# Kernel tuning notes

Hardware: AMD Instinct MI355X
Metric: run time of the kernel (lower is better)

Reference implementation:

```python
import jax, jax.numpy as jnp
import numpy as np

N_NODES = 100000
N_EDGES = 1600000
SZ_IN = 128
DIM_I = 1024


def setup_inputs() -> dict:
    key = jax.random.key(0)
    k1, k2, k3, k4, k5 = jax.random.split(key, 5)
    x = jax.random.normal(k1, (N_NODES, SZ_IN), dtype=jnp.float32)
    edge_index = jax.random.randint(k2, (2, N_EDGES), 0, N_NODES, dtype=jnp.int64)
    # torch Linear weight is [out_features, in_features]
    agg_W = jax.random.normal(k3, (SZ_IN, SZ_IN), dtype=jnp.float32) / np.sqrt(SZ_IN)
    agg_b = jnp.zeros((SZ_IN,), dtype=jnp.float32)
    lin_W = jax.random.normal(k4, (DIM_I, 2 * SZ_IN), dtype=jnp.float32) / np.sqrt(2 * SZ_IN)
    return {"x": x, "edge_index": edge_index, "agg_W": agg_W, "agg_b": agg_b, "lin_W": lin_W}


def reference(x, edge_index, agg_W, agg_b, lin_W):
    # GraphSAGE layer, depth=1, agg='max', concat=True, training mode (no self-loop/dropout edits).
    u, v = edge_index[0], edge_index[1]
    n = x.shape[0]
    # gather neighbor features, linear + ReLU  -> [E, sz_in]
    msg = jax.nn.relu(x[v] @ agg_W.T + agg_b)
    # scatter-max per target node; torch_scatter initializes out to zeros,
    # so missing nodes get 0 and all results are max(values, 0)
    hn = jnp.maximum(jax.ops.segment_max(msg, u, num_segments=n), 0.0)
    # concat + linear (no bias) + ReLU -> [N, dim_i]
    h = jax.nn.relu(jnp.concatenate([x, hn], axis=1) @ lin_W.T)
    return h
```

## Files before the change

kernel.cpp:

```cpp
#include <hip/hip_runtime.h>
#include <hip/hip_bf16.h>

typedef __attribute__((ext_vector_type(8))) short short8;
typedef __attribute__((ext_vector_type(4))) float f32x4;

__device__ __forceinline__ float bfu2f(unsigned short u) {
    unsigned int x = ((unsigned int)u) << 16;
    float f;
    __builtin_memcpy(&f, &x, 4);
    return f;
}
__device__ __forceinline__ unsigned short f2bfu(float f) {
    unsigned int x;
    __builtin_memcpy(&x, &f, 4);
    unsigned int r = (x + 0x7FFFu + ((x >> 16) & 1u)) >> 16;
    return (unsigned short)r;
}

__device__ __forceinline__ void gload_lds16(const void* g, void* l) {
    __builtin_amdgcn_global_load_lds(
        (const __attribute__((address_space(1))) void*)g,
        (__attribute__((address_space(3))) void*)l, 16, 0, 0);
}

#define BM 128
#define BN 128
#define BK 32
#define LDA 32
#define BCAP 64

template<bool F32OUT>
__device__ __forceinline__ void gemm_tile(
    const unsigned short* __restrict__ Alo,
    const unsigned short* __restrict__ Ahi,
    const unsigned short* __restrict__ B,
    const float* __restrict__ bias,
    void* __restrict__ Cv,
    int M, int N, int K, int relu, int m0, int n0,
    unsigned short* As, unsigned short* Bs)
{
    const int tid  = threadIdx.x;
    const int lane = tid & 63;
    const int wave = tid >> 6;
    const int wr   = wave >> 1;
    const int wc   = wave & 1;
    const int fm   = lane & 15;
    const int fq   = lane >> 4;

    f32x4 acc[4][4] = {};

    const int wbase = tid & ~63;

    for (int k0 = 0; k0 < K; k0 += BK) {
        __syncthreads();
        const unsigned short* Ab = (k0 < 128) ? Alo : Ahi;
        const int ka = (k0 < 128) ? k0 : (k0 - 128);
        #pragma unroll
        for (int i = 0; i < 2; ++i) {
            int c  = i * 256 + tid;
            int r  = c >> 2;
            int c8 = (c & 3) << 3;
            int grow = m0 + r;
            if (grow >= M) grow = M - 1;
            gload_lds16(Ab + (size_t)grow * 128 + ka + c8,
                        &As[(i * 256 + wbase) * 8]);
            gload_lds16(B + (size_t)(n0 + r) * K + k0 + c8,
                        &Bs[(i * 256 + wbase) * 8]);
        }
        __syncthreads();

        short8 af[4], bf[4];
        #pragma unroll
        for (int i = 0; i < 4; ++i)
            af[i] = *(const short8*)(&As[(wr * 64 + i * 16 + fm) * LDA + fq * 8]);
        #pragma unroll
        for (int j = 0; j < 4; ++j)
            bf[j] = *(const short8*)(&Bs[(wc * 64 + j * 16 + fm) * LDA + fq * 8]);

        #pragma unroll
        for (int i = 0; i < 4; ++i)
            #pragma unroll
            for (int j = 0; j < 4; ++j)
                acc[i][j] = __builtin_amdgcn_mfma_f32_16x16x32_bf16(
                                af[i], bf[j], acc[i][j], 0, 0, 0);
    }

    #pragma unroll
    for (int i = 0; i < 4; ++i) {
        #pragma unroll
        for (int r = 0; r < 4; ++r) {
            int gm = m0 + wr * 64 + i * 16 + fq * 4 + r;
            if (gm < M) {
                #pragma unroll
                for (int j = 0; j < 4; ++j) {
                    int gn = n0 + wc * 64 + j * 16 + fm;
                    float val = acc[i][j][r];
                    if (bias) val += bias[gn];
                    if (relu) val = fmaxf(val, 0.0f);
                    if (F32OUT)
                        __builtin_nontemporal_store(val,
                            &((float*)Cv)[(size_t)gm * N + gn]);
                    else
                        ((unsigned short*)Cv)[(size_t)gm * N + gn] = f2bfu(val);
                }
            }
        }
    }
}

template<bool F32OUT>
__global__ __launch_bounds__(256, 2)
void gemm_bt(const unsigned short* __restrict__ Alo,
             const unsigned short* __restrict__ Ahi,
             const unsigned short* __restrict__ B,
             const float* __restrict__ bias,
             void* __restrict__ Cv,
             int M, int N, int K, int relu)
{
    __shared__ unsigned short As[BM * LDA];
    __shared__ unsigned short Bs[BN * LDA];

    const int nwg  = gridDim.x * gridDim.y;
    int lid = blockIdx.y * gridDim.x + blockIdx.x;
    int wg  = lid;
    if ((nwg & 7) == 0) {
        int cpx = nwg >> 3;
        wg = (lid & 7) * cpx + (lid >> 3);
    }
    const int m0 = (wg / gridDim.x) * BM;
    const int n0 = (wg % gridDim.x) * BN;
    gemm_tile<F32OUT>(Alo, Ahi, B, bias, Cv, M, N, K, relu, m0, n0, As, Bs);
}

__global__ __launch_bounds__(256, 2)
void gemm1_fill_k(const unsigned short* __restrict__ xb,
                  const unsigned short* __restrict__ awb,
                  const float* __restrict__ bias,
                  unsigned short* __restrict__ y, int M, int MT,
                  const int* __restrict__ ei, int* __restrict__ cnt,
                  int* __restrict__ adj, int E)
{
    __shared__ unsigned short As[BM * LDA];
    __shared__ unsigned short Bs[BN * LDA];

    int b = blockIdx.x;
    if (b < MT) {
        gemm_tile<false>(xb, xb, awb, bias, y, M, 128, 128, 0, b * BM, 0, As, Bs);
        return;
    }
    int e = ((b - MT) * 256 + (int)threadIdx.x) * 4;
    if (e >= E) return;
    if (e + 3 < E) {
        int4 u = *(const int4*)(ei + e);
        int4 v = *(const int4*)(ei + E + e);
        int p0 = atomicAdd(&cnt[u.x], 1);
        int p1 = atomicAdd(&cnt[u.y], 1);
        int p2 = atomicAdd(&cnt[u.z], 1);
        int p3 = atomicAdd(&cnt[u.w], 1);
        if (p0 < BCAP) adj[((size_t)u.x << 6) + p0] = v.x;
        if (p1 < BCAP) adj[((size_t)u.y << 6) + p1] = v.y;
        if (p2 < BCAP) adj[((size_t)u.z << 6) + p2] = v.z;
        if (p3 < BCAP) adj[((size_t)u.w << 6) + p3] = v.w;
    } else {
        for (int j = 0; j < 4 && e + j < E; ++j) {
            int u = ei[e + j], v = ei[E + e + j];
            int p = atomicAdd(&cnt[u], 1);
            if (p < BCAP) adj[((size_t)u << 6) + p] = v;
        }
    }
}

__device__ __forceinline__ void cvt4(const float* __restrict__ src,
                                     unsigned short* __restrict__ dst, int t)
{
    float4 f = ((const float4*)src)[t];
    ushort4 o;
    o.x = f2bfu(f.x); o.y = f2bfu(f.y); o.z = f2bfu(f.z); o.w = f2bfu(f.w);
    ((ushort4*)dst)[t] = o;
}

__global__ __launch_bounds__(256)
void prep_k(const float* __restrict__ x, unsigned short* __restrict__ xb, int n4x,
            const float* __restrict__ aW, unsigned short* __restrict__ awb, int n4a,
            const float* __restrict__ lW, unsigned short* __restrict__ lwb, int n4l,
            int* __restrict__ cnt, int n4d)
{
    int t = blockIdx.x * 256 + threadIdx.x;
    if (t < n4x) { cvt4(x, xb, t); return; }
    t -= n4x;
    if (t < n4a) { cvt4(aW, awb, t); return; }
    t -= n4a;
    if (t < n4l) { cvt4(lW, lwb, t); return; }
    t -= n4l;
    if (t < n4d) ((int4*)cnt)[t] = make_int4(0, 0, 0, 0);
}

__global__ __launch_bounds__(256)
void gather_max_k(const int* __restrict__ cnt, const int* __restrict__ adj,
                  const unsigned short* __restrict__ y,
                  unsigned short* __restrict__ hnb, int NN)
{
    int t = blockIdx.x * 256 + threadIdx.x;
    int u = t >> 4;
    if (u >= NN) return;
    int c = (t & 15) << 3;
    const unsigned short* yc = y + c;
    int n = cnt[u];
    if (n > BCAP) n = BCAP;
    const int* bucket = adj + ((size_t)u << 6);
    short8 a0 = {0, 0, 0, 0, 0, 0, 0, 0};
    short8 a1 = {0, 0, 0, 0, 0, 0, 0, 0};
    int i = 0;
    for (; i + 3 < n; i += 4) {
        int v0 = bucket[i], v1 = bucket[i + 1], v2 = bucket[i + 2], v3 = bucket[i + 3];
        short8 y0 = *(const short8*)(yc + (size_t)v0 * 128);
        short8 y1 = *(const short8*)(yc + (size_t)v1 * 128);
        short8 y2 = *(const short8*)(yc + (size_t)v2 * 128);
        short8 y3 = *(const short8*)(yc + (size_t)v3 * 128);
        a0 = __builtin_elementwise_max(a0, y0);
        a1 = __builtin_elementwise_max(a1, y1);
        a0 = __builtin_elementwise_max(a0, y2);
        a1 = __builtin_elementwise_max(a1, y3);
    }
    for (; i < n; ++i) {
        short8 y0 = *(const short8*)(yc + (size_t)bucket[i] * 128);
        a0 = __builtin_elementwise_max(a0, y0);
    }
    a0 = __builtin_elementwise_max(a0, a1);
    *(short8*)(hnb + (size_t)u * 128 + c) = a0;
}

extern "C" void kernel_launch(void* const* d_in, const int* in_sizes, int n_in,
                              void* d_out, int out_size, void* d_ws, size_t ws_size,
                              hipStream_t stream)
{
    const float* x     = (const float*)d_in[0];
    const int*   ei    = (const int*)d_in[1];
    const float* agg_W = (const float*)d_in[2];
    const float* agg_b = (const float*)d_in[3];
    const float* lin_W = (const float*)d_in[4];
    float*       out   = (float*)d_out;

    const int NN = in_sizes[0] / 128;
    const int E  = in_sizes[1] / 2;
    const int DI = in_sizes[4] / 256;

    char* ws = (char*)d_ws;
    const size_t xN = (size_t)NN * 128;
    unsigned short* xb  = (unsigned short*)ws;
    unsigned short* y   = xb + xN;
    unsigned short* hnb = y + xN;
    unsigned short* awb = hnb + xN;
    unsigned short* lwb = awb + 128 * 128;
    char* p = (char*)(lwb + (size_t)DI * 256);
    int* cnt = (int*)p;
    int* adj = cnt + NN;

    const int MT = (NN + BM - 1) / BM;
    const int FB = (E / 4 + 255) / 256;

    const int n4x = (int)(xN / 4);
    const int n4a = 128 * 128 / 4;
    const int n4l = DI * 256 / 4;
    const int n4d = (NN + 3) / 4;
    {
        long long tot = (long long)n4x + n4a + n4l + n4d;
        prep_k<<<(int)((tot + 255) / 256), 256, 0, stream>>>(
            x, xb, n4x, agg_W, awb, n4a, lin_W, lwb, n4l, cnt, n4d);
    }

    gemm1_fill_k<<<MT + FB, 256, 0, stream>>>(xb, awb, agg_b, y, NN, MT,
                                              ei, cnt, adj, E);

    {
        long long threads = (long long)NN * 16;
        int blocks = (int)((threads + 255) / 256);
        gather_max_k<<<blocks, 256, 0, stream>>>(cnt, adj, y, hnb, NN);
    }

    gemm_bt<true><<<dim3(DI / BN, MT), 256, 0, stream>>>(xb, hnb, lwb, nullptr, out, NN, DI, 256, 1);
}
```

Before: 640.1 us.

## Replace final GEMM with 256x256-tile, 8-phase pipelined MFMA kernel

The output GEMM (N×256 by 256×1024, fp32 output) moves from the generic 128x128 tiled kernel to a dedicated 512-thread kernel. It uses 256x256 tiles, XOR-swizzled LDS with direct global-to-LDS loads, and an unrolled 8-phase schedule that overlaps staging of the next K-slice with MFMA work, using explicit waitcnt, barriers and setprio. The goal is more data reuse per tile and hiding of global-load latency in the dominant GEMM. In exchange the code is much more complex, LDS use per block rises, and the schedule is hardcoded for K=256.

```diff
diff --git a/kernel.cpp b/kernel.cpp
--- a/kernel.cpp
+++ b/kernel.cpp
@@ -48,7 +48,6 @@
     const int fq   = lane >> 4;
 
     f32x4 acc[4][4] = {};
-
     const int wbase = tid & ~63;
 
     for (int k0 = 0; k0 < K; k0 += BK) {
@@ -106,30 +105,6 @@
             }
         }
     }
-}
-
-template<bool F32OUT>
-__global__ __launch_bounds__(256, 2)
-void gemm_bt(const unsigned short* __restrict__ Alo,
-             const unsigned short* __restrict__ Ahi,
-             const unsigned short* __restrict__ B,
-             const float* __restrict__ bias,
-             void* __restrict__ Cv,
-             int M, int N, int K, int relu)
-{
-    __shared__ unsigned short As[BM * LDA];
-    __shared__ unsigned short Bs[BN * LDA];
-
-    const int nwg  = gridDim.x * gridDim.y;
-    int lid = blockIdx.y * gridDim.x + blockIdx.x;
-    int wg  = lid;
-    if ((nwg & 7) == 0) {
-        int cpx = nwg >> 3;
-        wg = (lid & 7) * cpx + (lid >> 3);
-    }
-    const int m0 = (wg / gridDim.x) * BM;
-    const int n0 = (wg % gridDim.x) * BN;
-    gemm_tile<F32OUT>(Alo, Ahi, B, bias, Cv, M, N, K, relu, m0, n0, As, Bs);
 }
 
 __global__ __launch_bounds__(256, 2)
@@ -168,6 +143,186 @@
             if (p < BCAP) adj[((size_t)u << 6) + p] = v;
         }
     }
+}
+
+#define BM2 256
+#define BN2 256
+
+__device__ __forceinline__ void stage_unit(const unsigned short* __restrict__ src,
+                                           int stride, int row0, int rmax,
+                                           unsigned short* dst, int tid)
+{
+    #pragma unroll
+    for (int j = 0; j < 2; ++j) {
+        int c = j * 512 + tid;
+        int r = c >> 3;
+        int s = (c & 7) ^ (r & 7);
+        int grow = row0 + r;
+        if (grow > rmax) grow = rmax;
+        gload_lds16(src + (size_t)grow * stride + s * 8,
+                    dst + (size_t)(j * 512 + (tid & ~63)) * 8);
+    }
+}
+
+__device__ __forceinline__ short8 frag_ld(const unsigned short* base, int row,
+                                          int ks, int fq)
+{
+    int cb = (ks * 64 + fq * 16) ^ ((row & 7) << 4);
+    return *(const short8*)((const char*)(base + row * 64) + cb);
+}
+
+__device__ __forceinline__ void load_a4(short8 (&a)[4][2],
+    const unsigned short* base, int wr, int fm, int fq)
+{
+    #pragma unroll
+    for (int mi = 0; mi < 4; ++mi)
+        #pragma unroll
+        for (int ks = 0; ks < 2; ++ks)
+            a[mi][ks] = frag_ld(base, wr * 64 + mi * 16 + fm, ks, fq);
+}
+__device__ __forceinline__ void load_b2(short8 (&bb)[2][2],
+    const unsigned short* base, int wc, int fm, int fq)
+{
+    #pragma unroll
+    for (int nj = 0; nj < 2; ++nj)
+        #pragma unroll
+        for (int ks = 0; ks < 2; ++ks)
+            bb[nj][ks] = frag_ld(base, wc * 32 + nj * 16 + fm, ks, fq);
+}
+
+#define PH_MID() do { \
+    __builtin_amdgcn_s_barrier(); \
+    asm volatile("s_waitcnt lgkmcnt(0)" ::: "memory"); \
+    __builtin_amdgcn_sched_barrier(0); \
+    __builtin_amdgcn_s_setprio(1); \
+} while (0)
+#define PH_END() do { \
+    __builtin_amdgcn_s_setprio(0); \
+    __builtin_amdgcn_s_barrier(); \
+    asm volatile("" ::: "memory"); \
+} while (0)
+
+template<int QM, int QN>
+__device__ __forceinline__ void do_mfma(f32x4 (&acc)[2][4][2][2],
+                                        short8 (&a)[4][2], short8 (&b)[2][2][2])
+{
+    #pragma unroll
+    for (int mi = 0; mi < 4; ++mi)
+        #pragma unroll
+        for (int nj = 0; nj < 2; ++nj)
+            #pragma unroll
+            for (int ks = 0; ks < 2; ++ks)
+                acc[QM][mi][QN][nj] = __builtin_amdgcn_mfma_f32_16x16x32_bf16(
+                    a[mi][ks], b[QN][nj][ks], acc[QM][mi][QN][nj], 0, 0, 0);
+}
+
+__global__ __launch_bounds__(512, 2)
+void gemm3_8ph(const unsigned short* __restrict__ xb,
+               const unsigned short* __restrict__ hnb,
+               const unsigned short* __restrict__ lwb,
+               float* __restrict__ out, int M, int N)
+{
+    __shared__ unsigned short lds[2][2][2][128 * 64];
+
+    const int tid = threadIdx.x;
+    const int nx  = gridDim.x;
+    const int nwg = nx * gridDim.y;
+    int orig = blockIdx.y * nx + blockIdx.x;
+    int q = nwg >> 3, r8 = nwg & 7;
+    int xcd = orig & 7, pos = orig >> 3;
+    int wg = (xcd < r8 ? xcd * (q + 1) : r8 * (q + 1) + (xcd - r8) * q) + pos;
+    const int m0 = (wg / nx) * BM2;
+    const int n0 = (wg % nx) * BN2;
+
+    const int lane = tid & 63;
+    const int wave = tid >> 6;
+    const int wr = wave >> 2;
+    const int wc = wave & 3;
+    const int fm = lane & 15;
+    const int fq = lane >> 4;
+    const int rmaxA = M - 1;
+    const int rmaxB = N - 1;
+
+    f32x4 acc[2][4][2][2] = {};
+    short8 a[4][2];
+    short8 b[2][2][2];
+
+    stage_unit(xb,        128, m0,        rmaxA, &lds[0][0][0][0], tid);
+    stage_unit(lwb,       256, n0,        rmaxB, &lds[0][1][0][0], tid);
+    stage_unit(lwb,       256, n0 + 128,  rmaxB, &lds[0][1][1][0], tid);
+    stage_unit(xb,        128, m0 + 128,  rmaxA, &lds[0][0][1][0], tid);
+    stage_unit(xb + 64,   128, m0,        rmaxA, &lds[1][0][0][0], tid);
+    stage_unit(lwb + 64,  256, n0,        rmaxB, &lds[1][1][0][0], tid);
+    stage_unit(lwb + 64,  256, n0 + 128,  rmaxB, &lds[1][1][1][0], tid);
+    asm volatile("s_waitcnt vmcnt(6)" ::: "memory");
+    __builtin_amdgcn_s_barrier();
+    asm volatile("" ::: "memory");
+
+    #pragma unroll
+    for (int it = 0; it < 2; ++it) {
+        const unsigned short* AT1 = (it == 0) ? xb + 64 : hnb + 64;
+
+        load_a4(a, &lds[0][0][0][0], wr, fm, fq);
+        load_b2(b[0], &lds[0][1][0][0], wc, fm, fq);
+        stage_unit(AT1, 128, m0 + 128, rmaxA, &lds[1][0][1][0], tid);
+        PH_MID(); do_mfma<0, 0>(acc, a, b); PH_END();
+
+        load_b2(b[1], &lds[0][1][1][0], wc, fm, fq);
+        if (it == 0) stage_unit(hnb, 128, m0, rmaxA, &lds[0][0][0][0], tid);
+        PH_MID(); do_mfma<0, 1>(acc, a, b); PH_END();
+
+        load_a4(a, &lds[0][0][1][0], wr, fm, fq);
+        if (it == 0) stage_unit(lwb + 128, 256, n0, rmaxB, &lds[0][1][0][0], tid);
+        PH_MID(); do_mfma<1, 0>(acc, a, b); PH_END();
+
+        if (it == 0) stage_unit(lwb + 128, 256, n0 + 128, rmaxB, &lds[0][1][1][0], tid);
+        PH_MID(); do_mfma<1, 1>(acc, a, b);
+        __builtin_amdgcn_s_setprio(0);
+        if (it == 0) asm volatile("s_waitcnt vmcnt(6)" ::: "memory");
+        else         asm volatile("s_waitcnt vmcnt(0)" ::: "memory");
+        __builtin_amdgcn_s_barrier();
+        asm volatile("" ::: "memory");
+
+        load_a4(a, &lds[1][0][0][0], wr, fm, fq);
+        load_b2(b[0], &lds[1][1][0][0], wc, fm, fq);
+        if (it == 0) stage_unit(hnb, 128, m0 + 128, rmaxA, &lds[0][0][1][0], tid);
+        PH_MID(); do_mfma<0, 0>(acc, a, b); PH_END();
+
+        load_b2(b[1], &lds[1][1][1][0], wc, fm, fq);
+        if (it == 0) stage_unit(hnb + 64, 128, m0, rmaxA, &lds[1][0][0][0], tid);
+        PH_MID(); do_mfma<0, 1>(acc, a, b); PH_END();
+
+        load_a4(a, &lds[1][0][1][0], wr, fm, fq);
+        if (it == 0) stage_unit(lwb + 192, 256, n0, rmaxB, &lds[1][1][0][0], tid);
+        PH_MID(); do_mfma<1, 0>(acc, a, b); PH_END();
+
+        if (it == 0) stage_unit(lwb + 192, 256, n0 + 128, rmaxB, &lds[1][1][1][0], tid);
+        PH_MID(); do_mfma<1, 1>(acc, a, b);
+        __builtin_amdgcn_s_setprio(0);
+        if (it == 0) asm volatile("s_waitcnt vmcnt(6)" ::: "memory");
+        __builtin_amdgcn_s_barrier();
+        asm volatile("" ::: "memory");
+    }
+
+    #pragma unroll
+    for (int qm = 0; qm < 2; ++qm)
+        #pragma unroll
+        for (int mi = 0; mi < 4; ++mi)
+            #pragma unroll
+            for (int rr = 0; rr < 4; ++rr) {
+                int gm = m0 + qm * 128 + wr * 64 + mi * 16 + fq * 4 + rr;
+                if (gm < M) {
+                    #pragma unroll
+                    for (int qn = 0; qn < 2; ++qn)
+                        #pragma unroll
+                        for (int nj = 0; nj < 2; ++nj) {
+                            int gn = n0 + qn * 128 + wc * 32 + nj * 16 + fm;
+                            float v = fmaxf(acc[qm][mi][qn][nj][rr], 0.0f);
+                            __builtin_nontemporal_store(v,
+                                &out[(size_t)gm * N + gn]);
+                        }
+                }
+            }
 }
 
 __device__ __forceinline__ void cvt4(const float* __restrict__ src,
@@ -278,5 +433,8 @@
         gather_max_k<<<blocks, 256, 0, stream>>>(cnt, adj, y, hnb, NN);
     }
 
-    gemm_bt<true><<<dim3(DI / BN, MT), 256, 0, stream>>>(xb, hnb, lwb, nullptr, out, NN, DI, 256, 1);
-}
+    {
+        dim3 g(DI / BN2, (NN + BM2 - 1) / BM2);
+        gemm3_8ph<<<g, 512, 0, stream>>>(xb, hnb, lwb, out, NN, DI);
+    }
+}
```

New measurement: 664.1 us. 1.04x slower.

## Fuse neighbor max-gather into final GEMM and drop hn buffer

Applied to the files above, without the earlier changes.

Removes the separate gather_max kernel and the hn intermediate: each block of the final GEMM gathers neighbor maxima for its 128 rows directly into LDS alongside the x tile, then sweeps all output column tiles reusing the A operand. The lin_W bf16 conversion is moved into the gemm1/fill launch. This saves a launch and an intermediate write and read. It risks lower occupancy from large LDS use and reduced parallelism, since one block now does all N tiles serially after a latency-bound gather.

```diff
diff --git a/kernel.cpp b/kernel.cpp
--- a/kernel.cpp
+++ b/kernel.cpp
@@ -4,12 +4,6 @@
 typedef __attribute__((ext_vector_type(8))) short short8;
 typedef __attribute__((ext_vector_type(4))) float f32x4;
 
-__device__ __forceinline__ float bfu2f(unsigned short u) {
-    unsigned int x = ((unsigned int)u) << 16;
-    float f;
-    __builtin_memcpy(&f, &x, 4);
-    return f;
-}
 __device__ __forceinline__ unsigned short f2bfu(float f) {
     unsigned int x;
     __builtin_memcpy(&x, &f, 4);
@@ -29,15 +23,12 @@
 #define LDA 32
 #define BCAP 64
 
-template<bool F32OUT>
-__device__ __forceinline__ void gemm_tile(
-    const unsigned short* __restrict__ Alo,
-    const unsigned short* __restrict__ Ahi,
+__device__ __forceinline__ void gemm_tile_bf16out(
+    const unsigned short* __restrict__ A,
     const unsigned short* __restrict__ B,
     const float* __restrict__ bias,
-    void* __restrict__ Cv,
-    int M, int N, int K, int relu, int m0, int n0,
-    unsigned short* As, unsigned short* Bs)
+    unsigned short* __restrict__ C,
+    int M, int m0, unsigned short* As, unsigned short* Bs)
 {
     const int tid  = threadIdx.x;
     const int lane = tid & 63;
@@ -48,13 +39,10 @@
     const int fq   = lane >> 4;
 
     f32x4 acc[4][4] = {};
-
     const int wbase = tid & ~63;
 
-    for (int k0 = 0; k0 < K; k0 += BK) {
+    for (int k0 = 0; k0 < 128; k0 += BK) {
         __syncthreads();
-        const unsigned short* Ab = (k0 < 128) ? Alo : Ahi;
-        const int ka = (k0 < 128) ? k0 : (k0 - 128);
         #pragma unroll
         for (int i = 0; i < 2; ++i) {
             int c  = i * 256 + tid;
@@ -62,9 +50,9 @@
             int c8 = (c & 3) << 3;
             int grow = m0 + r;
             if (grow >= M) grow = M - 1;
-            gload_lds16(Ab + (size_t)grow * 128 + ka + c8,
+            gload_lds16(A + (size_t)grow * 128 + k0 + c8,
                         &As[(i * 256 + wbase) * 8]);
-            gload_lds16(B + (size_t)(n0 + r) * K + k0 + c8,
+            gload_lds16(B + (size_t)r * 128 + k0 + c8,
                         &Bs[(i * 256 + wbase) * 8]);
         }
         __syncthreads();
@@ -93,43 +81,22 @@
             if (gm < M) {
                 #pragma unroll
                 for (int j = 0; j < 4; ++j) {
-                    int gn = n0 + wc * 64 + j * 16 + fm;
-                    float val = acc[i][j][r];
-                    if (bias) val += bias[gn];
-                    if (relu) val = fmaxf(val, 0.0f);
-                    if (F32OUT)
-                        __builtin_nontemporal_store(val,
-                            &((float*)Cv)[(size_t)gm * N + gn]);
-                    else
-                        ((unsigned short*)Cv)[(size_t)gm * N + gn] = f2bfu(val);
+                    int gn = wc * 64 + j * 16 + fm;
+                    float val = acc[i][j][r] + bias[gn];
+                    C[(size_t)gm * 128 + gn] = f2bfu(val);
                 }
             }
         }
     }
 }
 
-template<bool F32OUT>
-__global__ __launch_bounds__(256, 2)
-void gemm_bt(const unsigned short* __restrict__ Alo,
-             const unsigned short* __restrict__ Ahi,
-             const unsigned short* __restrict__ B,
-             const float* __restrict__ bias,
-             void* __restrict__ Cv,
-             int M, int N, int K, int relu)
-{
-    __shared__ unsigned short As[BM * LDA];
-    __shared__ unsigned short Bs[BN * LDA];
-
-    const int nwg  = gridDim.x * gridDim.y;
-    int lid = blockIdx.y * gridDim.x + blockIdx.x;
-    int wg  = lid;
-    if ((nwg & 7) == 0) {
-        int cpx = nwg >> 3;
-        wg = (lid & 7) * cpx + (lid >> 3);
-    }
-    const int m0 = (wg / gridDim.x) * BM;
-    const int n0 = (wg % gridDim.x) * BN;
-    gemm_tile<F32OUT>(Alo, Ahi, B, bias, Cv, M, N, K, relu, m0, n0, As, Bs);
+__device__ __forceinline__ void cvt4(const float* __restrict__ src,
+                                     unsigned short* __restrict__ dst, int t)
+{
+    float4 f = ((const float4*)src)[t];
+    ushort4 o;
+    o.x = f2bfu(f.x); o.y = f2bfu(f.y); o.z = f2bfu(f.z); o.w = f2bfu(f.w);
+    ((ushort4*)dst)[t] = o;
 }
 
 __global__ __launch_bounds__(256, 2)
@@ -138,51 +105,48 @@
                   const float* __restrict__ bias,
                   unsigned short* __restrict__ y, int M, int MT,
                   const int* __restrict__ ei, int* __restrict__ cnt,
-                  int* __restrict__ adj, int E)
+                  int* __restrict__ adj, int E, int FB,
+                  const float* __restrict__ lW,
+                  unsigned short* __restrict__ lwb, int n4l)
 {
     __shared__ unsigned short As[BM * LDA];
     __shared__ unsigned short Bs[BN * LDA];
 
     int b = blockIdx.x;
     if (b < MT) {
-        gemm_tile<false>(xb, xb, awb, bias, y, M, 128, 128, 0, b * BM, 0, As, Bs);
+        gemm_tile_bf16out(xb, awb, bias, y, M, b * BM, As, Bs);
         return;
     }
-    int e = ((b - MT) * 256 + (int)threadIdx.x) * 4;
-    if (e >= E) return;
-    if (e + 3 < E) {
-        int4 u = *(const int4*)(ei + e);
-        int4 v = *(const int4*)(ei + E + e);
-        int p0 = atomicAdd(&cnt[u.x], 1);
-        int p1 = atomicAdd(&cnt[u.y], 1);
-        int p2 = atomicAdd(&cnt[u.z], 1);
-        int p3 = atomicAdd(&cnt[u.w], 1);
-        if (p0 < BCAP) adj[((size_t)u.x << 6) + p0] = v.x;
-        if (p1 < BCAP) adj[((size_t)u.y << 6) + p1] = v.y;
-        if (p2 < BCAP) adj[((size_t)u.z << 6) + p2] = v.z;
-        if (p3 < BCAP) adj[((size_t)u.w << 6) + p3] = v.w;
-    } else {
-        for (int j = 0; j < 4 && e + j < E; ++j) {
-            int u = ei[e + j], v = ei[E + e + j];
-            int p = atomicAdd(&cnt[u], 1);
-            if (p < BCAP) adj[((size_t)u << 6) + p] = v;
-        }
-    }
-}
-
-__device__ __forceinline__ void cvt4(const float* __restrict__ src,
-                                     unsigned short* __restrict__ dst, int t)
-{
-    float4 f = ((const float4*)src)[t];
-    ushort4 o;
-    o.x = f2bfu(f.x); o.y = f2bfu(f.y); o.z = f2bfu(f.z); o.w = f2bfu(f.w);
-    ((ushort4*)dst)[t] = o;
+    if (b < MT + FB) {
+        int e = ((b - MT) * 256 + (int)threadIdx.x) * 4;
+        if (e >= E) return;
+        if (e + 3 < E) {
+            int4 u = *(const int4*)(ei + e);
+            int4 v = *(const int4*)(ei + E + e);
+            int p0 = atomicAdd(&cnt[u.x], 1);
+            int p1 = atomicAdd(&cnt[u.y], 1);
+            int p2 = atomicAdd(&cnt[u.z], 1);
+            int p3 = atomicAdd(&cnt[u.w], 1);
+            if (p0 < BCAP) adj[((size_t)u.x << 6) + p0] = v.x;
+            if (p1 < BCAP) adj[((size_t)u.y << 6) + p1] = v.y;
+            if (p2 < BCAP) adj[((size_t)u.z << 6) + p2] = v.z;
+            if (p3 < BCAP) adj[((size_t)u.w << 6) + p3] = v.w;
+        } else {
+            for (int j = 0; j < 4 && e + j < E; ++j) {
+                int u = ei[e + j], v = ei[E + e + j];
+                int p = atomicAdd(&cnt[u], 1);
+                if (p < BCAP) adj[((size_t)u << 6) + p] = v;
+            }
+        }
+        return;
+    }
+    int t = (b - MT - FB) * 256 + (int)threadIdx.x;
+    if (t < n4l) cvt4(lW, lwb, t);
 }
 
 __global__ __launch_bounds__(256)
 void prep_k(const float* __restrict__ x, unsigned short* __restrict__ xb, int n4x,
             const float* __restrict__ aW, unsigned short* __restrict__ awb, int n4a,
-            const float* __restrict__ lW, unsigned short* __restrict__ lwb, int n4l,
             int* __restrict__ cnt, int n4d)
 {
     int t = blockIdx.x * 256 + threadIdx.x;
@@ -190,44 +154,131 @@
     t -= n4x;
     if (t < n4a) { cvt4(aW, awb, t); return; }
     t -= n4a;
-    if (t < n4l) { cvt4(lW, lwb, t); return; }
-    t -= n4l;
     if (t < n4d) ((int4*)cnt)[t] = make_int4(0, 0, 0, 0);
 }
 
-__global__ __launch_bounds__(256)
-void gather_max_k(const int* __restrict__ cnt, const int* __restrict__ adj,
-                  const unsigned short* __restrict__ y,
-                  unsigned short* __restrict__ hnb, int NN)
-{
-    int t = blockIdx.x * 256 + threadIdx.x;
-    int u = t >> 4;
-    if (u >= NN) return;
-    int c = (t & 15) << 3;
-    const unsigned short* yc = y + c;
-    int n = cnt[u];
-    if (n > BCAP) n = BCAP;
-    const int* bucket = adj + ((size_t)u << 6);
-    short8 a0 = {0, 0, 0, 0, 0, 0, 0, 0};
-    short8 a1 = {0, 0, 0, 0, 0, 0, 0, 0};
-    int i = 0;
-    for (; i + 3 < n; i += 4) {
-        int v0 = bucket[i], v1 = bucket[i + 1], v2 = bucket[i + 2], v3 = bucket[i + 3];
-        short8 y0 = *(const short8*)(yc + (size_t)v0 * 128);
-        short8 y1 = *(const short8*)(yc + (size_t)v1 * 128);
-        short8 y2 = *(const short8*)(yc + (size_t)v2 * 128);
-        short8 y3 = *(const short8*)(yc + (size_t)v3 * 128);
-        a0 = __builtin_elementwise_max(a0, y0);
-        a1 = __builtin_elementwise_max(a1, y1);
-        a0 = __builtin_elementwise_max(a0, y2);
-        a1 = __builtin_elementwise_max(a1, y3);
-    }
-    for (; i < n; ++i) {
-        short8 y0 = *(const short8*)(yc + (size_t)bucket[i] * 128);
-        a0 = __builtin_elementwise_max(a0, y0);
-    }
-    a0 = __builtin_elementwise_max(a0, a1);
-    *(short8*)(hnb + (size_t)u * 128 + c) = a0;
+__global__ __launch_bounds__(256, 2)
+void gemm3_fused(const unsigned short* __restrict__ xb,
+                 const unsigned short* __restrict__ lwb,
+                 const int* __restrict__ cnt,
+                 const int* __restrict__ adj,
+                 const unsigned short* __restrict__ y,
+                 float* __restrict__ out, int M, int N)
+{
+    __shared__ unsigned short Ah[8][128 * 32];
+    __shared__ unsigned short Bs[128 * 32];
+
+    const int tid = threadIdx.x;
+    const int m0  = blockIdx.x * 128;
+    const int wbase = tid & ~63;
+
+    #pragma unroll
+    for (int kc = 0; kc < 4; ++kc) {
+        #pragma unroll
+        for (int i = 0; i < 2; ++i) {
+            int c  = i * 256 + tid;
+            int r  = c >> 2;
+            int c8 = (c & 3) << 3;
+            int grow = m0 + r;
+            if (grow >= M) grow = M - 1;
+            gload_lds16(xb + (size_t)grow * 128 + kc * 32 + c8,
+                        &Ah[kc][(i * 256 + wbase) * 8]);
+        }
+    }
+
+    {
+        int g   = tid >> 4;
+        int ch  = (tid & 15) << 3;
+        int kc  = 4 + (ch >> 5);
+        int col = ch & 31;
+        const unsigned short* yc = y + ch;
+        for (int p = 0; p < 8; ++p) {
+            int r = p * 16 + g;
+            int u = m0 + r;
+            short8 a0 = {0, 0, 0, 0, 0, 0, 0, 0};
+            short8 a1 = {0, 0, 0, 0, 0, 0, 0, 0};
+            if (u < M) {
+                int n = cnt[u];
+                if (n > BCAP) n = BCAP;
+                const int* bucket = adj + ((size_t)u << 6);
+                int i = 0;
+                for (; i + 3 < n; i += 4) {
+                    int v0 = bucket[i],     v1 = bucket[i + 1];
+                    int v2 = bucket[i + 2], v3 = bucket[i + 3];
+                    short8 y0 = *(const short8*)(yc + (size_t)v0 * 128);
+                    short8 y1 = *(const short8*)(yc + (size_t)v1 * 128);
+                    short8 y2 = *(const short8*)(yc + (size_t)v2 * 128);
+                    short8 y3 = *(const short8*)(yc + (size_t)v3 * 128);
+                    a0 = __builtin_elementwise_max(a0, y0);
+                    a1 = __builtin_elementwise_max(a1, y1);
+                    a0 = __builtin_elementwise_max(a0, y2);
+                    a1 = __builtin_elementwise_max(a1, y3);
+                }
+                for (; i < n; ++i) {
+                    short8 y0 = *(const short8*)(yc + (size_t)bucket[i] * 128);
+                    a0 = __builtin_elementwise_max(a0, y0);
+                }
+            }
+            a0 = __builtin_elementwise_max(a0, a1);
+            *(short8*)(&Ah[kc][r * 32 + col]) = a0;
+        }
+    }
+    __syncthreads();
+
+    const int lane = tid & 63;
+    const int wave = tid >> 6;
+    const int wr   = wave >> 1;
+    const int wc   = wave & 1;
+    const int fm   = lane & 15;
+    const int fq   = lane >> 4;
+
+    for (int j = 0; j < N / BN; ++j) {
+        int n0 = j * BN;
+        f32x4 acc[4][4] = {};
+        for (int kc = 0; kc < 8; ++kc) {
+            __syncthreads();
+            #pragma unroll
+            for (int i = 0; i < 2; ++i) {
+                int c  = i * 256 + tid;
+                int r  = c >> 2;
+                int c8 = (c & 3) << 3;
+                gload_lds16(lwb + (size_t)(n0 + r) * 256 + kc * 32 + c8,
+                            &Bs[(i * 256 + wbase) * 8]);
+            }
+            __syncthreads();
+
+            short8 af[4], bf[4];
+            #pragma unroll
+            for (int i = 0; i < 4; ++i)
+                af[i] = *(const short8*)(&Ah[kc][(wr * 64 + i * 16 + fm) * LDA + fq * 8]);
+            #pragma unroll
+            for (int j2 = 0; j2 < 4; ++j2)
+                bf[j2] = *(const short8*)(&Bs[(wc * 64 + j2 * 16 + fm) * LDA + fq * 8]);
+
+            #pragma unroll
+            for (int i = 0; i < 4; ++i)
+                #pragma unroll
+                for (int j2 = 0; j2 < 4; ++j2)
+                    acc[i][j2] = __builtin_amdgcn_mfma_f32_16x16x32_bf16(
+                                     af[i], bf[j2], acc[i][j2], 0, 0, 0);
+        }
+
+        #pragma unroll
+        for (int i = 0; i < 4; ++i) {
+            #pragma unroll
+            for (int r = 0; r < 4; ++r) {
+                int gm = m0 + wr * 64 + i * 16 + fq * 4 + r;
+                if (gm < M) {
+                    #pragma unroll
+                    for (int j2 = 0; j2 < 4; ++j2) {
+                        int gn = n0 + wc * 64 + j2 * 16 + fm;
+                        float v = fmaxf(acc[i][j2][r], 0.0f);
+                        __builtin_nontemporal_store(v, &out[(size_t)gm * N + gn]);
+                    }
+                }
+            }
+        }
+    }
 }
 
 extern "C" void kernel_launch(void* const* d_in, const int* in_sizes, int n_in,
@@ -249,8 +300,7 @@
     const size_t xN = (size_t)NN * 128;
     unsigned short* xb  = (unsigned short*)ws;
     unsigned short* y   = xb + xN;
-    unsigned short* hnb = y + xN;
-    unsigned short* awb = hnb + xN;
+    unsigned short* awb = y + xN;
     unsigned short* lwb = awb + 128 * 128;
     char* p = (char*)(lwb + (size_t)DI * 256);
     int* cnt = (int*)p;
@@ -258,25 +308,21 @@
 
     const int MT = (NN + BM - 1) / BM;
     const int FB = (E / 4 + 255) / 256;
+    const int n4l = DI * 256 / 4;
+    const int LB = (n4l + 255) / 256;
 
     const int n4x = (int)(xN / 4);
     const int n4a = 128 * 128 / 4;
-    const int n4l = DI * 256 / 4;
     const int n4d = (NN + 3) / 4;
     {
-        long long tot = (long long)n4x + n4a + n4l + n4d;
+        long long tot = (long long)n4x + n4a + n4d;
         prep_k<<<(int)((tot + 255) / 256), 256, 0, stream>>>(
-            x, xb, n4x, agg_W, awb, n4a, lin_W, lwb, n4l, cnt, n4d);
-    }
-
-    gemm1_fill_k<<<MT + FB, 256, 0, stream>>>(xb, awb, agg_b, y, NN, MT,
-                                              ei, cnt, adj, E);
-
-    {
-        long long threads = (long long)NN * 16;
-        int blocks = (int)((threads + 255) / 256);
-        gather_max_k<<<blocks, 256, 0, stream>>>(cnt, adj, y, hnb, NN);
-    }
-
-    gemm_bt<true><<<dim3(DI / BN, MT), 256, 0, stream>>>(xb, hnb, lwb, nullptr, out, NN, DI, 256, 1);
-}
+            x, xb, n4x, agg_W, awb, n4a, cnt, n4d);
+    }
+
+    gemm1_fill_k<<<MT + FB + LB, 256, 0, stream>>>(xb, awb, agg_b, y, NN, MT,
+                                                   ei, cnt, adj, E, FB,
+                                                   lin_W, lwb, n4l);
+
+    gemm3_fused<<<MT, 256, 0, stream>>>(xb, lwb, cnt, adj, y, out, NN, DI);
+}
```

Measured after the change: 706.1 us. 1.1x slower.
